# Kernel optimization log

Measured on AMD Instinct MI355X. Metric: run time of the kernel, lower is better.

Reference implementation:

```python
import jax, jax.numpy as jnp
import numpy as np
import math

D_MODEL = 2048
N_HEADS = 16
D_K = D_MODEL // N_HEADS


def setup_inputs() -> dict:
    key = jax.random.key(0)
    k0, k1, k2, k3, k4 = jax.random.split(key, 5)
    B, T = 2, 2048
    x = jax.random.normal(k0, (B, T, D_MODEL), dtype=jnp.float32)
    s = 1.0 / math.sqrt(D_MODEL)
    W_qkv = jax.random.normal(k1, (3 * D_MODEL, D_MODEL), dtype=jnp.float32) * s
    b_qkv = jax.random.normal(k2, (3 * D_MODEL,), dtype=jnp.float32) * 0.01
    W_out = jax.random.normal(k3, (D_MODEL, D_MODEL), dtype=jnp.float32) * s
    b_out = jax.random.normal(k4, (D_MODEL,), dtype=jnp.float32) * 0.01
    return {"x": x, "W_qkv": W_qkv, "b_qkv": b_qkv, "W_out": W_out, "b_out": b_out}


def reference(x, W_qkv, b_qkv, W_out, b_out):
    B, T, C = x.shape
    qkv = x @ W_qkv.T + b_qkv                      # [B,T,3C]
    q, k, v = jnp.split(qkv, 3, axis=-1)
    # [B,T,C] -> [B,H,T,Dk]
    def to_heads(t):
        return t.reshape(B, T, N_HEADS, D_K).transpose(0, 2, 1, 3)
    q, k, v = to_heads(q), to_heads(k), to_heads(v)
    scale = 1.0 / math.sqrt(D_K)
    scores = jnp.einsum('bhqd,bhkd->bhqk', q, k) * scale   # [B,H,T,T]
    causal = jnp.tril(jnp.ones((T, T), dtype=bool))
    neg = jnp.finfo(scores.dtype).min
    scores = jnp.where(causal[None, None], scores, neg)
    attn = jax.nn.softmax(scores, axis=-1)
    out = jnp.einsum('bhqk,bhkd->bhqd', attn, v)           # [B,H,T,Dk]
    out = out.transpose(0, 2, 1, 3).reshape(B, T, C)
    return out @ W_out.T + b_out
```

## Files before the change

### kernel.cpp

```cpp
#include <hip/hip_runtime.h>
#include <stdint.h>

typedef short bf16x8 __attribute__((ext_vector_type(8)));
typedef float f32x4 __attribute__((ext_vector_type(4)));
typedef float f32x16 __attribute__((ext_vector_type(16)));
typedef unsigned short u16;
typedef unsigned int u32;

__device__ __forceinline__ u16 f2bf(float f) {
    u32 x = __float_as_uint(f);
    x += 0x7fffu + ((x >> 16) & 1u);
    return (u16)(x >> 16);
}
__device__ __forceinline__ u32 pack_bf2(float a, float b) {
    return (u32)f2bf(a) | ((u32)f2bf(b) << 16);
}

union Frag4 { u32 u[4]; bf16x8 v; };

__device__ __forceinline__ void gload16(const u16* g, u16* l) {
    __builtin_amdgcn_global_load_lds(
        (__attribute__((address_space(1))) void*)g,
        (__attribute__((address_space(3))) void*)l,
        16, 0, 0);
}

__global__ void cvt_f32_bf16(const float* __restrict__ in, u16* __restrict__ out, long n8) {
    long stride = (long)gridDim.x * blockDim.x;
    for (long i = (long)blockIdx.x * blockDim.x + threadIdx.x; i < n8; i += stride) {
        const float4* p = (const float4*)(in + i * 8);
        float4 a = p[0], b = p[1];
        uint4 o;
        o.x = pack_bf2(a.x, a.y);
        o.y = pack_bf2(a.z, a.w);
        o.z = pack_bf2(b.x, b.y);
        o.w = pack_bf2(b.z, b.w);
        ((uint4*)out)[i] = o;
    }
}

template<int OBF>
__global__ __launch_bounds__(256, 2) void gemm_nt(
    const u16* __restrict__ A, const u16* __restrict__ B,
    const float* __restrict__ bias, void* __restrict__ out,
    int K, int ldo, int gxsh)
{
    __shared__ __align__(16) u16 lA[2 * 128 * 64];
    __shared__ __align__(16) u16 lB[2 * 128 * 64];
    const int tid  = threadIdx.x;
    const int lane = tid & 63;
    const int w    = tid >> 6;
    const int wm = (w >> 1) * 64, wn = (w & 1) * 64;

    const int nwg = gridDim.x;
    const int bid = blockIdx.x;
    const int swz = (bid & 7) * (nwg >> 3) + (bid >> 3);
    const int bm = (swz & ((1 << gxsh) - 1)) * 128;
    const int bn = (swz >> gxsh) * 128;

    const int lr = lane >> 3;
    const u32 sb = (u32)((lane & 7) * 16);
    const int NT = K >> 6;

    auto stage = [&](int bb, int k0) {
#pragma unroll
        for (int i = 0; i < 4; ++i) {
            const int c = w * 4 + i;
            const int row = c * 8 + lr;
            const u32 col = (sb ^ ((u32)(row & 7) << 4)) >> 1;
            gload16(A + (size_t)(bm + row) * K + k0 + col, lA + bb * 8192 + c * 512);
            gload16(B + (size_t)(bn + row) * K + k0 + col, lB + bb * 8192 + c * 512);
        }
    };

    f32x4 acc[4][4];
#pragma unroll
    for (int i = 0; i < 4; ++i)
#pragma unroll
        for (int j = 0; j < 4; ++j)
#pragma unroll
            for (int r = 0; r < 4; ++r) acc[i][j][r] = 0.f;

    stage(0, 0);
    stage(1, 64);
    asm volatile("s_waitcnt vmcnt(8)" ::: "memory");
    __builtin_amdgcn_sched_barrier(0);
    __builtin_amdgcn_s_barrier();
    __builtin_amdgcn_sched_barrier(0);

    for (int t = 0; t < NT; ++t) {
        const int cur = t & 1;
        const char* pA = (const char*)(lA + cur * 8192);
        const char* pB = (const char*)(lB + cur * 8192);
#pragma unroll
        for (int kk = 0; kk < 2; ++kk) {
            bf16x8 af[4], bfr[4];
#pragma unroll
            for (int f = 0; f < 4; ++f) {
                const int m = wm + f * 16 + (lane & 15);
                const u32 byt = (u32)(kk * 64 + (lane >> 4) * 16) ^ ((u32)(m & 7) << 4);
                af[f]  = *(const bf16x8*)(pA + m * 128 + byt);
                const int n = wn + f * 16 + (lane & 15);
                const u32 bytb = (u32)(kk * 64 + (lane >> 4) * 16) ^ ((u32)(n & 7) << 4);
                bfr[f] = *(const bf16x8*)(pB + n * 128 + bytb);
            }
            __builtin_amdgcn_s_setprio(1);
#pragma unroll
            for (int i = 0; i < 4; ++i)
#pragma unroll
                for (int j = 0; j < 4; ++j)
                    acc[i][j] = __builtin_amdgcn_mfma_f32_16x16x32_bf16(af[i], bfr[j], acc[i][j], 0, 0, 0);
            __builtin_amdgcn_s_setprio(0);
        }
        __builtin_amdgcn_sched_barrier(0);
        __builtin_amdgcn_s_barrier();
        __builtin_amdgcn_sched_barrier(0);
        if (t + 2 < NT) {
            stage(cur, (t + 2) * 64);
            asm volatile("s_waitcnt vmcnt(8)" ::: "memory");
        } else {
            asm volatile("s_waitcnt vmcnt(0)" ::: "memory");
        }
        __builtin_amdgcn_sched_barrier(0);
        __builtin_amdgcn_s_barrier();
        __builtin_amdgcn_sched_barrier(0);
    }

#pragma unroll
    for (int i = 0; i < 4; ++i) {
        int m0 = bm + wm + i * 16 + ((lane >> 4) << 2);
#pragma unroll
        for (int j = 0; j < 4; ++j) {
            int n = bn + wn + j * 16 + (lane & 15);
            float bv = bias[n];
#pragma unroll
            for (int r = 0; r < 4; ++r) {
                float v = acc[i][j][r] + bv;
                if constexpr (OBF != 0)
                    ((u16*)out)[(size_t)(m0 + r) * ldo + n] = f2bf(v);
                else
                    ((float*)out)[(size_t)(m0 + r) * ldo + n] = v;
            }
        }
    }
}

__global__ __launch_bounds__(256) void transpose_v(
    const u16* __restrict__ qkv, u16* __restrict__ vt)
{
    __shared__ u16 lt[64 * 64];
    const int tid = threadIdx.x;
    const int bid = blockIdx.x;
    const int tt    = bid & 31;
    const int dtile = (bid >> 5) & 1;
    const int h     = (bid >> 6) & 15;
    const int b     = bid >> 10;
    const u16* src = qkv + ((size_t)b * 2048 + tt * 64) * 6144 + 4096 + h * 128 + dtile * 64;

    const int r = tid >> 2, ce = (tid & 3) * 16;
    uint4 a0 = *(const uint4*)(src + (size_t)r * 6144 + ce);
    uint4 a1 = *(const uint4*)(src + (size_t)r * 6144 + ce + 8);
    const u32 swz = (u32)((r & 7) << 4);
    *(uint4*)((char*)lt + r * 128 + (((u32)(ce * 2)) ^ swz)) = a0;
    *(uint4*)((char*)lt + r * 128 + (((u32)(ce * 2 + 16)) ^ swz)) = a1;
    __syncthreads();

    const int d = tid >> 2;
    u16* dst = vt + ((size_t)(b * 16 + h) * 128 + dtile * 64 + d) * 2048 + tt * 64;
#pragma unroll
    for (int it = 0; it < 2; ++it) {
        const int t0 = (tid & 3) * 8 + it * 32;
        union { u16 hh[8]; uint4 q4; } u;
#pragma unroll
        for (int uu = 0; uu < 8; ++uu) {
            int trow = t0 + uu;
            u32 byt = (u32)(trow * 128) + (((u32)(d * 2)) ^ ((u32)((trow & 7) << 4)));
            u.hh[uu] = *(const u16*)((const char*)lt + byt);
        }
        *(uint4*)(dst + t0) = u.q4;
    }
}

__global__ __launch_bounds__(256) void attn_fwd(
    const u16* __restrict__ qkv, const u16* __restrict__ vt,
    u16* __restrict__ obuf)
{
    __shared__ __align__(16) u16 lK[2 * 64 * 128];
    __shared__ __align__(16) u16 lV[2 * 128 * 64];
    const int tid  = threadIdx.x;
    const int lane = tid & 63;
    const int w    = tid >> 6;
    const int g    = lane >> 5;
    const int ql   = lane & 31;

    const int bid = blockIdx.x;
    const int qi  = bid >> 5;
    const int bh  = bid & 31;
    const int qtile = (qi < 8) ? (15 - qi) : (qi - 8);
    const int b = bh >> 4, h = bh & 15;
    const size_t rowbase = (size_t)b * 2048;
    const int qb = qtile * 128;
    const int qw = qb + w * 32;
    const int q  = qw + ql;
    const int nt = 2 * qtile + 2;

    const u16* Khead = qkv + rowbase * 6144 + 2048 + h * 128;
    const u16* Vth   = vt + (size_t)bh * 128 * 2048;

    bf16x8 qf[8];
    {
        const u16* qrow = qkv + (rowbase + q) * 6144 + h * 128;
#pragma unroll
        for (int ch = 0; ch < 8; ++ch)
            qf[ch] = *(const bf16x8*)(qrow + ch * 16 + g * 8);
    }

    f32x16 acc[4];
#pragma unroll
    for (int dt = 0; dt < 4; ++dt)
#pragma unroll
        for (int r = 0; r < 16; ++r) acc[dt][r] = 0.f;

    float m_run = -1e30f, l_run = 0.f;
    const float C2 = 0.08838834764831845f * 1.44269504088896341f;

    auto stage = [&](int bb, int t) {
        const int kb = t * 64;
#pragma unroll
        for (int i = 0; i < 4; ++i) {
            const int c = w * 4 + i;
            const int kr = c * 4 + (lane >> 4);
            const u32 kcol = (((u32)((lane & 15) * 16)) ^ ((u32)(kr & 7) << 4)) >> 1;
            gload16(Khead + (size_t)(kb + kr) * 6144 + kcol,
                    lK + bb * 8192 + c * 512);
            const int vr = c * 8 + (lane >> 3);
            const u32 vcol = (((u32)((lane & 7) * 16)) ^ ((u32)(vr & 7) << 4)) >> 1;
            gload16(Vth + (size_t)vr * 2048 + kb + vcol,
                    lV + bb * 8192 + c * 512);
        }
    };

    stage(0, 0);
    __syncthreads();
    int buf = 0;

    for (int t = 0; t < nt; ++t) {
        const int kb = t * 64;
        if (t + 1 < nt) stage(buf ^ 1, t + 1);

        if (kb <= qw + 31) {
            const char* lKb = (const char*)(lK + buf * 8192);
            const char* lVb = (const char*)(lV + buf * 8192);
#pragma unroll
            for (int s = 0; s < 2; ++s) {
                const int kb2 = kb + s * 32;
                if (kb2 > qw + 31) break;
                const bool diag = (kb2 == qw);

                bf16x8 kf[8];
                const u32 krow = (u32)(s * 32 + ql);
                const u32 ksw = (krow & 7) << 4;
#pragma unroll
                for (int ch = 0; ch < 8; ++ch)
                    kf[ch] = *(const bf16x8*)(lKb + krow * 256 + (((u32)(ch * 32 + g * 16)) ^ ksw));

                f32x16 s_;
#pragma unroll
                for (int r = 0; r < 16; ++r) s_[r] = 0.f;
                __builtin_amdgcn_s_setprio(1);
#pragma unroll
                for (int ch = 0; ch < 8; ++ch)
                    s_ = __builtin_amdgcn_mfma_f32_32x32x16_bf16(kf[ch], qf[ch], s_, 0, 0, 0);
                __builtin_amdgcn_s_setprio(0);

                float p[16];
                float tmax = -1e30f;
#pragma unroll
                for (int r = 0; r < 16; ++r) {
                    int crow = (r & 3) + 8 * (r >> 2) + 4 * g;
                    float v = s_[r];
                    if (diag && (crow > ql)) v = -1e30f;
                    p[r] = v;
                    tmax = fmaxf(tmax, v);
                }
                tmax = fmaxf(tmax, __shfl_xor(tmax, 32));
                if (!__all(tmax <= m_run + 8.0f)) {
                    float mnew  = fmaxf(m_run, tmax);
                    float alpha = exp2f((m_run - mnew) * C2);
#pragma unroll
                    for (int dt = 0; dt < 4; ++dt) acc[dt] = acc[dt] * alpha;
                    l_run *= alpha;
                    m_run = mnew;
                }
                float ssum = 0.f;
#pragma unroll
                for (int r = 0; r < 16; ++r) {
                    float e = exp2f((p[r] - m_run) * C2);
                    p[r] = e;
                    ssum += e;
                }
                ssum += __shfl_xor(ssum, 32);
                l_run += ssum;

                u32 wb[8], sw[8];
#pragma unroll
                for (int j = 0; j < 8; ++j) wb[j] = pack_bf2(p[2 * j], p[2 * j + 1]);
#pragma unroll
                for (int j = 0; j < 8; ++j) sw[j] = __shfl_xor(wb[j], 32);
                Frag4 pf0, pf1;
#pragma unroll
                for (int u = 0; u < 4; ++u) {
                    const bool own = (g == (u >> 1));
                    pf0.u[u] = own ? wb[2 * g + (u & 1)]     : sw[2 * g + (u & 1)];
                    pf1.u[u] = own ? wb[4 + 2 * g + (u & 1)] : sw[4 + 2 * g + (u & 1)];
                }

                __builtin_amdgcn_s_setprio(1);
#pragma unroll
                for (int dt = 0; dt < 4; ++dt) {
                    const u32 vrow = (u32)(dt * 32 + ql);
                    const u32 vsw = (vrow & 7) << 4;
                    bf16x8 v0 = *(const bf16x8*)(lVb + vrow * 128 + (((u32)(s * 64 + g * 16)) ^ vsw));
                    bf16x8 v1 = *(const bf16x8*)(lVb + vrow * 128 + (((u32)(s * 64 + 32 + g * 16)) ^ vsw));
                    acc[dt] = __builtin_amdgcn_mfma_f32_32x32x16_bf16(v0, pf0.v, acc[dt], 0, 0, 0);
                    acc[dt] = __builtin_amdgcn_mfma_f32_32x32x16_bf16(v1, pf1.v, acc[dt], 0, 0, 0);
                }
                __builtin_amdgcn_s_setprio(0);
            }
        }
        __syncthreads();
        buf ^= 1;
    }

    const float inv_l = 1.0f / l_run;
    u16* orow = obuf + (rowbase + q) * 2048 + h * 128;
#pragma unroll
    for (int dt = 0; dt < 4; ++dt) {
#pragma unroll
        for (int rr = 0; rr < 4; ++rr) {
            int d0 = dt * 32 + rr * 8 + g * 4;
            int r0 = rr * 4;
            u32 w0 = pack_bf2(acc[dt][r0] * inv_l,     acc[dt][r0 + 1] * inv_l);
            u32 w1 = pack_bf2(acc[dt][r0 + 2] * inv_l, acc[dt][r0 + 3] * inv_l);
            *(u32*)(orow + d0)     = w0;
            *(u32*)(orow + d0 + 2) = w1;
        }
    }
}

extern "C" void kernel_launch(void* const* d_in, const int* in_sizes, int n_in,
                              void* d_out, int out_size, void* d_ws, size_t ws_size,
                              hipStream_t stream) {
    (void)in_sizes; (void)n_in; (void)out_size; (void)ws_size;
    const float* x    = (const float*)d_in[0];
    const float* Wqkv = (const float*)d_in[1];
    const float* bqkv = (const float*)d_in[2];
    const float* Wout = (const float*)d_in[3];
    const float* bout = (const float*)d_in[4];

    char* ws = (char*)d_ws;
    u16* xb  = (u16*)ws;
    u16* wqb = (u16*)(ws + (size_t)16777216);
    u16* qkv = (u16*)(ws + (size_t)41943040);
    u16* ob  = xb;
    u16* vtb = wqb;
    u16* wob = wqb;

    cvt_f32_bf16<<<2048, 256, 0, stream>>>(x, xb, 8388608L / 8);
    cvt_f32_bf16<<<2048, 256, 0, stream>>>(Wqkv, wqb, 12582912L / 8);
    gemm_nt<1><<<1536, 256, 0, stream>>>(xb, wqb, bqkv, qkv, 2048, 6144, 5);
    transpose_v<<<2048, 256, 0, stream>>>(qkv, vtb);
    attn_fwd<<<512, 256, 0, stream>>>(qkv, vtb, ob);
    cvt_f32_bf16<<<2048, 256, 0, stream>>>(Wout, wob, 4194304L / 8);
    gemm_nt<0><<<512, 256, 0, stream>>>(ob, wob, bout, d_out, 2048, 2048, 5);
}
```

Measured before the change: 349.8 us.

## Split long causal attention query tiles across two blocks and merge partials

Measured after the change: 347.7 us. No clear change (-0.6%).

```diff
diff --git a/kernel.cpp b/kernel.cpp
--- a/kernel.cpp
+++ b/kernel.cpp
@@ -181,9 +181,12 @@
     }
 }
 
+__constant__ unsigned char QT_TAB[24] = {15,15,7,14,14,13,13,6,12,12,11,11,5,10,10,9,9,4,8,8,3,2,1,0};
+__constant__ unsigned char CK_TAB[24] = {0,1,2,0,1,0,1,2,0,1,0,1,2,0,1,0,1,2,0,1,2,2,2,2};
+
 __global__ __launch_bounds__(256) void attn_fwd(
     const u16* __restrict__ qkv, const u16* __restrict__ vt,
-    u16* __restrict__ obuf)
+    u16* __restrict__ obuf, float* __restrict__ pout, float* __restrict__ pml)
 {
     __shared__ __align__(16) u16 lK[2 * 64 * 128];
     __shared__ __align__(16) u16 lV[2 * 128 * 64];
@@ -193,16 +196,18 @@
     const int g    = lane >> 5;
     const int ql   = lane & 31;
 
-    const int bid = blockIdx.x;
-    const int qi  = bid >> 5;
-    const int bh  = bid & 31;
-    const int qtile = (qi < 8) ? (15 - qi) : (qi - 8);
+    const int bid  = blockIdx.x;
+    const int item = bid >> 5;
+    const int bh   = bid & 31;
+    const int qt   = QT_TAB[item];
+    const int ck   = CK_TAB[item];
     const int b = bh >> 4, h = bh & 15;
     const size_t rowbase = (size_t)b * 2048;
-    const int qb = qtile * 128;
+    const int qb = qt * 128;
     const int qw = qb + w * 32;
     const int q  = qw + ql;
-    const int nt = 2 * qtile + 2;
+    const int t_lo = (ck == 1) ? (qt + 1) : 0;
+    const int t_hi = (ck == 0) ? (qt + 1) : (2 * qt + 2);
 
     const u16* Khead = qkv + rowbase * 6144 + 2048 + h * 128;
     const u16* Vth   = vt + (size_t)bh * 128 * 2048;
@@ -240,13 +245,13 @@
         }
     };
 
-    stage(0, 0);
+    stage(0, t_lo);
     __syncthreads();
     int buf = 0;
 
-    for (int t = 0; t < nt; ++t) {
+    for (int t = t_lo; t < t_hi; ++t) {
         const int kb = t * 64;
-        if (t + 1 < nt) stage(buf ^ 1, t + 1);
+        if (t + 1 < t_hi) stage(buf ^ 1, t + 1);
 
         if (kb <= qw + 31) {
             const char* lKb = (const char*)(lK + buf * 8192);
@@ -332,19 +337,76 @@
         buf ^= 1;
     }
 
-    const float inv_l = 1.0f / l_run;
-    u16* orow = obuf + (rowbase + q) * 2048 + h * 128;
-#pragma unroll
-    for (int dt = 0; dt < 4; ++dt) {
-#pragma unroll
-        for (int rr = 0; rr < 4; ++rr) {
-            int d0 = dt * 32 + rr * 8 + g * 4;
-            int r0 = rr * 4;
-            u32 w0 = pack_bf2(acc[dt][r0] * inv_l,     acc[dt][r0 + 1] * inv_l);
-            u32 w1 = pack_bf2(acc[dt][r0 + 2] * inv_l, acc[dt][r0 + 3] * inv_l);
-            *(u32*)(orow + d0)     = w0;
-            *(u32*)(orow + d0 + 2) = w1;
-        }
+    if (ck == 2) {
+        const float inv_l = 1.0f / l_run;
+        u16* orow = obuf + (rowbase + q) * 2048 + h * 128;
+#pragma unroll
+        for (int dt = 0; dt < 4; ++dt) {
+#pragma unroll
+            for (int rr = 0; rr < 4; ++rr) {
+                int d0 = dt * 32 + rr * 8 + g * 4;
+                int r0 = rr * 4;
+                u32 w0 = pack_bf2(acc[dt][r0] * inv_l,     acc[dt][r0 + 1] * inv_l);
+                u32 w1 = pack_bf2(acc[dt][r0 + 2] * inv_l, acc[dt][r0 + 3] * inv_l);
+                *(u32*)(orow + d0)     = w0;
+                *(u32*)(orow + d0 + 2) = w1;
+            }
+        }
+    } else {
+        const int slot = (((bh << 3) | (qt - 8)) << 1) + ck;
+        const int qloc = w * 32 + ql;
+        float* po = pout + (size_t)slot * 16384 + (size_t)qloc * 128;
+#pragma unroll
+        for (int dt = 0; dt < 4; ++dt) {
+#pragma unroll
+            for (int rr = 0; rr < 4; ++rr) {
+                int d0 = dt * 32 + rr * 8 + g * 4;
+                int r0 = rr * 4;
+                float4 v4 = make_float4(acc[dt][r0], acc[dt][r0 + 1],
+                                        acc[dt][r0 + 2], acc[dt][r0 + 3]);
+                *(float4*)(po + d0) = v4;
+            }
+        }
+        if (g == 0) {
+            float2* pm = (float2*)pml + slot * 128 + qloc;
+            *pm = make_float2(m_run, l_run);
+        }
+    }
+}
+
+__global__ __launch_bounds__(256) void attn_merge(
+    const float* __restrict__ pout, const float* __restrict__ pml,
+    u16* __restrict__ obuf)
+{
+    const int bid = blockIdx.x;
+    const int bh = bid >> 3, qto = bid & 7;
+    const int b = bh >> 4, h = bh & 15;
+    const int tid = threadIdx.x;
+    const int qloc = tid >> 1, half = (tid & 1) * 64;
+    const int base = ((bh << 3) | qto) << 1;
+    const float C2 = 0.08838834764831845f * 1.44269504088896341f;
+
+    const float2 ml0 = ((const float2*)pml)[(base + 0) * 128 + qloc];
+    const float2 ml1 = ((const float2*)pml)[(base + 1) * 128 + qloc];
+    const float ms = fmaxf(ml0.x, ml1.x);
+    const float w0 = exp2f((ml0.x - ms) * C2);
+    const float w1 = exp2f((ml1.x - ms) * C2);
+    const float inv = 1.0f / (ml0.y * w0 + ml1.y * w1);
+
+    const float* p0 = pout + (size_t)(base + 0) * 16384 + (size_t)qloc * 128 + half;
+    const float* p1 = pout + (size_t)(base + 1) * 16384 + (size_t)qloc * 128 + half;
+    const int qrow = (8 + qto) * 128 + qloc;
+    u16* orow = obuf + ((size_t)b * 2048 + qrow) * 2048 + h * 128 + half;
+#pragma unroll
+    for (int j = 0; j < 64; j += 4) {
+        float4 a = *(const float4*)(p0 + j);
+        float4 c = *(const float4*)(p1 + j);
+        float o0 = (a.x * w0 + c.x * w1) * inv;
+        float o1 = (a.y * w0 + c.y * w1) * inv;
+        float o2 = (a.z * w0 + c.z * w1) * inv;
+        float o3 = (a.w * w0 + c.w * w1) * inv;
+        *(u32*)(orow + j)     = pack_bf2(o0, o1);
+        *(u32*)(orow + j + 2) = pack_bf2(o2, o3);
     }
 }
 
@@ -365,12 +427,15 @@
     u16* ob  = xb;
     u16* vtb = wqb;
     u16* wob = wqb;
+    float* pml = (float*)(ws + (size_t)33554432);
+    float* pO  = (float*)d_out;
 
     cvt_f32_bf16<<<2048, 256, 0, stream>>>(x, xb, 8388608L / 8);
     cvt_f32_bf16<<<2048, 256, 0, stream>>>(Wqkv, wqb, 12582912L / 8);
     gemm_nt<1><<<1536, 256, 0, stream>>>(xb, wqb, bqkv, qkv, 2048, 6144, 5);
     transpose_v<<<2048, 256, 0, stream>>>(qkv, vtb);
-    attn_fwd<<<512, 256, 0, stream>>>(qkv, vtb, ob);
+    attn_fwd<<<768, 256, 0, stream>>>(qkv, vtb, ob, pO, pml);
+    attn_merge<<<256, 256, 0, stream>>>(pO, pml, ob);
     cvt_f32_bf16<<<2048, 256, 0, stream>>>(Wout, wob, 4194304L / 8);
     gemm_nt<0><<<512, 256, 0, stream>>>(ob, wob, bout, d_out, 2048, 2048, 5);
 }
```
